# Kernel tuning notes

Hardware: AMD Instinct MI355X
Metric: run time of the kernel (lower is better)

The kernel has to match this reference:

```python
import jax, jax.numpy as jnp
import numpy as np
import math

N = 50000
E = 500000
IN_C = 128
T_FEAT = 16
OUT_C = 128
EPS = 1e-5
NEG_SLOPE = 0.01


def setup_inputs() -> dict:
    key = jax.random.key(0)
    ks = jax.random.split(key, 10)
    x = jax.random.normal(ks[0], (N, IN_C), dtype=jnp.float32)
    edge_index = jax.random.randint(ks[1], (2, E), 0, N, dtype=jnp.int64)
    edge_weight = jax.random.uniform(ks[2], (E,), dtype=jnp.float32)
    time_diff = jax.random.uniform(ks[3], (1,), dtype=jnp.float32)
    d_in = IN_C + T_FEAT
    morning_freq = jax.random.normal(ks[4], (T_FEAT,), dtype=jnp.float32)
    W_gcn = jax.random.normal(ks[5], (d_in, OUT_C), dtype=jnp.float32) / np.sqrt(d_in)
    b_gcn = jnp.zeros((OUT_C,), dtype=jnp.float32)
    gamma = jnp.ones((OUT_C,), dtype=jnp.float32)
    beta = jnp.zeros((OUT_C,), dtype=jnp.float32)
    W_lin = jax.random.normal(ks[6], (OUT_C, OUT_C), dtype=jnp.float32) / np.sqrt(OUT_C)
    b_lin = jax.random.normal(ks[7], (OUT_C,), dtype=jnp.float32) * 0.01
    return {"x": x, "edge_index": edge_index, "edge_weight": edge_weight,
            "time_diff": time_diff, "morning_freq": morning_freq,
            "W_gcn": W_gcn, "b_gcn": b_gcn, "gamma": gamma, "beta": beta,
            "W_lin": W_lin, "b_lin": b_lin}


def _gcn_conv(h, edge_index, edge_weight):
    # PyG GCNConv aggregation: add self-loops (weight 1), symmetric normalization.
    row, col = edge_index[0], edge_index[1]
    loop = jnp.arange(N, dtype=edge_index.dtype)
    row_f = jnp.concatenate([row, loop])
    col_f = jnp.concatenate([col, loop])
    ew_f = jnp.concatenate([edge_weight, jnp.ones((N,), dtype=h.dtype)])
    deg = jax.ops.segment_sum(ew_f, col_f, num_segments=N)
    dinv = jnp.where(deg > 0, jax.lax.rsqrt(jnp.maximum(deg, 1e-12)), 0.0)
    norm = dinv[row_f] * ew_f * dinv[col_f]                 # [E+N]
    msg = h[row_f] * norm[:, None]                          # gather + scale
    return jax.ops.segment_sum(msg, col_f, num_segments=N)  # scatter-add


def reference(x, edge_index, edge_weight, time_diff, morning_freq,
              W_gcn, b_gcn, gamma, beta, W_lin, b_lin):
    td = time_diff[0]
    # time_segment == 'morning_peak': sin encoding, tiled over all nodes
    enc = jnp.sin(td * morning_freq * math.pi)              # [T]
    enc = jnp.broadcast_to(enc[None, :], (x.shape[0], T_FEAT))
    h = jnp.concatenate([x, enc], axis=1)                   # [N, in+T]
    h = h @ W_gcn                                           # GCN linear transform
    h = _gcn_conv(h, edge_index, edge_weight) + b_gcn       # [N, out]
    # BatchNorm1d (training-mode batch statistics, biased variance)
    mean = jnp.mean(h, axis=0)
    var = jnp.mean(jnp.square(h - mean), axis=0)
    h = gamma * (h - mean) * jax.lax.rsqrt(var + EPS) + beta
    h = jnp.where(h >= 0, h, NEG_SLOPE * h)                 # LeakyReLU
    h = h @ W_lin + b_lin                                   # Linear (dropout=eval identity)
    return h
```

## Files before the change

### kernel.cpp

```cpp
#include <hip/hip_runtime.h>
#include <hip/hip_bf16.h>

#define NN 50000
#define NE 500000
#define C 128
#define NBLK ((NN + 255) / 256)
#define HISTB ((NE + 255) / 256)
#define SPB (NN / 8)
#define RB 128
#define RROWS ((SPB + RB - 1) / RB)
#define GB ((NN + 63) / 64)
#define BN_EPS 1e-5f
#define NEG 0.01f
#define WSCALE 16777216.0f
#define WMASK  0xFFFFFFFFFFFULL

typedef __attribute__((ext_vector_type(8))) short bf16x8;
typedef __attribute__((ext_vector_type(4))) float f32x4;

__device__ inline unsigned short f2bf(float f) {
    unsigned int u = __float_as_uint(f);
    unsigned int r = (u + 0x7fffu + ((u >> 16) & 1u)) >> 16;
    return (unsigned short)r;
}
__device__ inline unsigned int pack2(float a, float b) {
    return (unsigned int)f2bf(a) | ((unsigned int)f2bf(b) << 16);
}
__device__ inline float4 bf4_to_f4(uint2 u) {
    float4 r;
    r.x = __uint_as_float(u.x << 16);
    r.y = __uint_as_float(u.x & 0xffff0000u);
    r.z = __uint_as_float(u.y << 16);
    r.w = __uint_as_float(u.y & 0xffff0000u);
    return r;
}

__global__ __launch_bounds__(256) void setup_kernel(const float* __restrict__ Wg,
                                                    const float* __restrict__ Wl,
                                                    unsigned int* __restrict__ Wgt,
                                                    unsigned int* __restrict__ Wlt,
                                                    const float* __restrict__ td,
                                                    const float* __restrict__ mf,
                                                    float* __restrict__ cvec,
                                                    float* __restrict__ zreg) {
    const int b = blockIdx.x;
    const int t = threadIdx.x;
    if (b < 128) {
        long i = (long)b * 256 + t;
        const long n = 2L * NN + 4;
        const long s = 128L * 256;
        for (; i < n; i += s) zreg[i] = 0.f;
    } else if (b == 128) {
        const int col = t >> 1;
        const int half = t & 1;
        for (int j = 0; j < 32; j++) {
            int ku = half * 32 + j;
            int k0 = 2 * ku;
            unsigned int g = (unsigned int)((ku >> 2) ^ (col & 15));
            unsigned int slot = (unsigned int)col * 64u + (g << 2) + (unsigned int)(ku & 3);
            Wgt[slot] = pack2(Wg[(size_t)k0 * C + col], Wg[(size_t)(k0 + 1) * C + col]);
            Wlt[slot] = pack2(Wl[(size_t)k0 * C + col], Wl[(size_t)(k0 + 1) * C + col]);
        }
    } else {
        if (t < 128) {
            float tv = td[0];
            float acc = 0.f;
#pragma unroll
            for (int j = 0; j < 16; j++) {
                float s = sinf(tv * mf[j] * 3.14159265358979323846f);
                acc = fmaf(s, Wg[(128 + j) * C + t], acc);
            }
            cvec[t] = acc;
        }
    }
}

__global__ void hist_kernel(const int* __restrict__ ei, const float* __restrict__ ew,
                            unsigned long long* __restrict__ hist, int* __restrict__ rank) {
    int e = blockIdx.x * blockDim.x + threadIdx.x;
    if (e < NE) {
        int c = ei[NE + e];
        unsigned long long pack = (1ULL << 44) | (unsigned long long)(ew[e] * WSCALE);
        unsigned long long old = atomicAdd(&hist[c], pack);
        rank[e] = (int)(old >> 44);
    }
}

__global__ __launch_bounds__(256) void gemm1_kernel(const float* __restrict__ X,
                                                    const unsigned int* __restrict__ Wt,
                                                    const float* __restrict__ cvec,
                                                    unsigned short* __restrict__ Hb) {
    __shared__ unsigned int wsh[8192];
    const int t = threadIdx.x;
#pragma unroll
    for (int i = 0; i < 8; i++)
        ((uint4*)wsh)[t + i * 256] = ((const uint4*)Wt)[t + i * 256];

    const int lane = t & 63;
    const int wid = t >> 6;
    const int lrow = lane & 15;
    const int kb = lane >> 4;
    const int row = blockIdx.x * 64 + wid * 16 + lrow;
    const float* xrow = X + (size_t)min(row, NN - 1) * C;

    f32x4 acc[8];
#pragma unroll
    for (int n = 0; n < 8; n++) acc[n] = (f32x4){0.f, 0.f, 0.f, 0.f};
    __syncthreads();

#pragma unroll
    for (int ks = 0; ks < 4; ks++) {
        float4 a0 = *(const float4*)(xrow + ks * 32 + kb * 8);
        float4 a1 = *(const float4*)(xrow + ks * 32 + kb * 8 + 4);
        union { unsigned int u[4]; bf16x8 v; } af;
        af.u[0] = pack2(a0.x, a0.y); af.u[1] = pack2(a0.z, a0.w);
        af.u[2] = pack2(a1.x, a1.y); af.u[3] = pack2(a1.z, a1.w);
        const unsigned int gp = (unsigned int)((ks * 4 + kb) ^ lrow);
#pragma unroll
        for (int n = 0; n < 8; n++) {
            int col = n * 16 + lrow;
            union { uint4 q; bf16x8 v; } bfm;
            bfm.q = *(const uint4*)&wsh[col * 64 + gp * 4];
            acc[n] = __builtin_amdgcn_mfma_f32_16x16x32_bf16(af.v, bfm.v, acc[n], 0, 0, 0);
        }
    }
    const int orow = blockIdx.x * 64 + wid * 16 + kb * 4;
#pragma unroll
    for (int n = 0; n < 8; n++) {
        int col = n * 16 + lrow;
        float cv = cvec[col];
#pragma unroll
        for (int i = 0; i < 4; i++) {
            int r = orow + i;
            if (r < NN) Hb[(size_t)r * C + col] = f2bf(acc[n][i] + cv);
        }
    }
}

__global__ __launch_bounds__(256) void scanp1_kernel(const unsigned long long* __restrict__ hist,
                                                     int* __restrict__ rptr,
                                                     int* __restrict__ bsum) {
    __shared__ int s[256];
    const int t = threadIdx.x;
    const int i = blockIdx.x * 256 + t;
    int v = (i < NN) ? (int)(hist[i] >> 44) : 0;
    s[t] = v;
    __syncthreads();
    for (int off = 1; off < 256; off <<= 1) {
        int add = (t >= off) ? s[t - off] : 0;
        __syncthreads();
        s[t] += add;
        __syncthreads();
    }
    if (i < NN) rptr[i] = s[t] - v;
    if (t == 255) bsum[blockIdx.x] = s[255];
}

__global__ __launch_bounds__(256) void scanp3_kernel(int* __restrict__ rptr,
                                                     const int* __restrict__ bsum,
                                                     const unsigned long long* __restrict__ hist,
                                                     float* __restrict__ dinv) {
    __shared__ int sb[256];
    const int t = threadIdx.x;
    const int b = blockIdx.x;
    sb[t] = (t < NBLK && t < b) ? bsum[t] : 0;
    __syncthreads();
    for (int off = 128; off > 0; off >>= 1) {
        if (t < off) sb[t] += sb[t + off];
        __syncthreads();
    }
    const int boff = sb[0];
    const int i = b * 256 + t;
    if (i < NN) {
        rptr[i] += boff;
        float degw = (float)(hist[i] & WMASK) * (1.0f / WSCALE);
        dinv[i] = rsqrtf(degw + 1.0f);
    }
    if (b == 0 && t == 0) rptr[NN] = NE;
}

__global__ void fill_kernel(const int* __restrict__ ei, const float* __restrict__ ew,
                            const float* __restrict__ dinv, const int* __restrict__ rptr,
                            const int* __restrict__ rank, int2* __restrict__ csr) {
    int e = blockIdx.x * blockDim.x + threadIdx.x;
    if (e >= NE) return;
    int r = ei[e], c = ei[NE + e];
    int slot = rptr[c] + rank[e];
    float w = dinv[r] * ew[e] * dinv[c];
    csr[slot] = make_int2(r, __float_as_int(w));
}

__global__ __launch_bounds__(256) void spmm_kernel(const int* __restrict__ rptr,
                                                   const int2* __restrict__ csr,
                                                   const unsigned short* __restrict__ Hb,
                                                   const float* __restrict__ dinv,
                                                   const float* __restrict__ bg,
                                                   float* __restrict__ OUT,
                                                   float* __restrict__ P) {
    const int nl = threadIdx.x >> 5;
    const int lane = threadIdx.x & 31;
    const int node = blockIdx.x * 8 + nl;
    const int ch = lane * 4;
    int s = rptr[node], e = rptr[node + 1];
    float d = dinv[node];
    float dd = d * d;
    float4 h = bf4_to_f4(*(const uint2*)(Hb + (size_t)node * C + ch));
    float4 acc = make_float4(dd * h.x, dd * h.y, dd * h.z, dd * h.w);
    float4 accB = make_float4(0.f, 0.f, 0.f, 0.f);
    int j = s;
    for (; j + 4 <= e; j += 4) {
        int2 e0 = csr[j], e1 = csr[j + 1], e2 = csr[j + 2], e3 = csr[j + 3];
        float w0 = __int_as_float(e0.y), w1 = __int_as_float(e1.y);
        float w2 = __int_as_float(e2.y), w3 = __int_as_float(e3.y);
        uint2 u0 = *(const uint2*)(Hb + (size_t)e0.x * C + ch);
        uint2 u1 = *(const uint2*)(Hb + (size_t)e1.x * C + ch);
        uint2 u2 = *(const uint2*)(Hb + (size_t)e2.x * C + ch);
        uint2 u3 = *(const uint2*)(Hb + (size_t)e3.x * C + ch);
        float4 v0 = bf4_to_f4(u0), v1 = bf4_to_f4(u1), v2 = bf4_to_f4(u2), v3 = bf4_to_f4(u3);
        acc.x = fmaf(v0.x, w0, acc.x);  acc.y = fmaf(v0.y, w0, acc.y);
        acc.z = fmaf(v0.z, w0, acc.z);  acc.w = fmaf(v0.w, w0, acc.w);
        accB.x = fmaf(v1.x, w1, accB.x); accB.y = fmaf(v1.y, w1, accB.y);
        accB.z = fmaf(v1.z, w1, accB.z); accB.w = fmaf(v1.w, w1, accB.w);
        acc.x = fmaf(v2.x, w2, acc.x);  acc.y = fmaf(v2.y, w2, acc.y);
        acc.z = fmaf(v2.z, w2, acc.z);  acc.w = fmaf(v2.w, w2, acc.w);
        accB.x = fmaf(v3.x, w3, accB.x); accB.y = fmaf(v3.y, w3, accB.y);
        accB.z = fmaf(v3.z, w3, accB.z); accB.w = fmaf(v3.w, w3, accB.w);
    }
    for (; j < e; j++) {
        int2 e0 = csr[j];
        float w0 = __int_as_float(e0.y);
        float4 v0 = bf4_to_f4(*(const uint2*)(Hb + (size_t)e0.x * C + ch));
        acc.x = fmaf(v0.x, w0, acc.x); acc.y = fmaf(v0.y, w0, acc.y);
        acc.z = fmaf(v0.z, w0, acc.z); acc.w = fmaf(v0.w, w0, acc.w);
    }
    acc.x += accB.x; acc.y += accB.y; acc.z += accB.z; acc.w += accB.w;
    float4 b = *(const float4*)(bg + ch);
    acc.x += b.x; acc.y += b.y; acc.z += b.z; acc.w += b.w;
    *(float4*)(OUT + (size_t)node * C + ch) = acc;

    __shared__ __align__(16) float4 sred[2][8][32];
    float4 sq = make_float4(acc.x * acc.x, acc.y * acc.y, acc.z * acc.z, acc.w * acc.w);
    sred[0][nl][lane] = acc;
    sred[1][nl][lane] = sq;
    __syncthreads();
    if (nl == 0) {
        float4 s0 = sred[0][0][lane], q0 = sred[1][0][lane];
#pragma unroll
        for (int k = 1; k < 8; k++) {
            float4 a = sred[0][k][lane];
            float4 q = sred[1][k][lane];
            s0.x += a.x; s0.y += a.y; s0.z += a.z; s0.w += a.w;
            q0.x += q.x; q0.y += q.y; q0.z += q.z; q0.w += q.w;
        }
        float* row = P + (size_t)blockIdx.x * 256;
        *(float4*)(row + ch) = s0;
        *(float4*)(row + 128 + ch) = q0;
    }
}

__global__ __launch_bounds__(256) void reduce1_kernel(const float* __restrict__ P,
                                                      float* __restrict__ P2,
                                                      unsigned int* __restrict__ cnt,
                                                      const float* __restrict__ gm,
                                                      const float* __restrict__ bt,
                                                      float* __restrict__ sc,
                                                      float* __restrict__ sh) {
    const int c = threadIdx.x;
    const int r0 = blockIdx.x * RROWS;
    const int r1 = min(r0 + RROWS, SPB);
    float a0 = 0.f, a1 = 0.f, a2 = 0.f, a3 = 0.f;
    int r = r0;
    for (; r + 4 <= r1; r += 4) {
        a0 += P[(size_t)(r + 0) * 256 + c];
        a1 += P[(size_t)(r + 1) * 256 + c];
        a2 += P[(size_t)(r + 2) * 256 + c];
        a3 += P[(size_t)(r + 3) * 256 + c];
    }
    for (; r < r1; r++) a0 += P[(size_t)r * 256 + c];
    P2[(size_t)blockIdx.x * 256 + c] = (a0 + a1) + (a2 + a3);

    __threadfence();
    __shared__ unsigned int done;
    if (c == 0) done = atomicAdd(cnt, 1u);
    __syncthreads();
    if (done == RB - 1) {
        __threadfence();
        if (c < 128) {
            float s0 = 0.f, s1 = 0.f, q0 = 0.f, q1 = 0.f;
            for (int k = 0; k < RB; k += 2) {
                s0 += P2[(size_t)k * 256 + c];
                q0 += P2[(size_t)k * 256 + 128 + c];
                s1 += P2[(size_t)(k + 1) * 256 + c];
                q1 += P2[(size_t)(k + 1) * 256 + 128 + c];
            }
            float ssum = s0 + s1, ssq = q0 + q1;
            float mean = ssum / (float)NN;
            float var = ssq / (float)NN - mean * mean;
            var = fmaxf(var, 0.f);
            float rs = rsqrtf(var + BN_EPS);
            float s = gm[c] * rs;
            sc[c] = s;
            sh[c] = bt[c] - mean * s;
        }
    }
}

__global__ __launch_bounds__(256) void final_kernel(float* __restrict__ OUT,
                                                    const unsigned int* __restrict__ Wt,
                                                    const float* __restrict__ bl,
                                                    const float* __restrict__ sc,
                                                    const float* __restrict__ sh) {
    __shared__ unsigned int wsh[8192];
    const int t = threadIdx.x;
#pragma unroll
    for (int i = 0; i < 8; i++)
        ((uint4*)wsh)[t + i * 256] = ((const uint4*)Wt)[t + i * 256];

    const int lane = t & 63;
    const int wid = t >> 6;
    const int lrow = lane & 15;
    const int kb = lane >> 4;
    const int row = blockIdx.x * 64 + wid * 16 + lrow;
    const float* hrow = OUT + (size_t)min(row, NN - 1) * C;

    f32x4 acc[8];
#pragma unroll
    for (int n = 0; n < 8; n++) acc[n] = (f32x4){0.f, 0.f, 0.f, 0.f};
    __syncthreads();

#pragma unroll
    for (int ks = 0; ks < 4; ks++) {
        const int k0 = ks * 32 + kb * 8;
        float4 v0 = *(const float4*)(hrow + k0);
        float4 v1 = *(const float4*)(hrow + k0 + 4);
        float4 s0 = *(const float4*)(sc + k0);
        float4 s1 = *(const float4*)(sc + k0 + 4);
        float4 h0 = *(const float4*)(sh + k0);
        float4 h1 = *(const float4*)(sh + k0 + 4);
        float a[8];
        a[0] = fmaf(v0.x, s0.x, h0.x); a[1] = fmaf(v0.y, s0.y, h0.y);
        a[2] = fmaf(v0.z, s0.z, h0.z); a[3] = fmaf(v0.w, s0.w, h0.w);
        a[4] = fmaf(v1.x, s1.x, h1.x); a[5] = fmaf(v1.y, s1.y, h1.y);
        a[6] = fmaf(v1.z, s1.z, h1.z); a[7] = fmaf(v1.w, s1.w, h1.w);
#pragma unroll
        for (int i = 0; i < 8; i++) a[i] = a[i] >= 0.f ? a[i] : NEG * a[i];
        union { unsigned int u[4]; bf16x8 v; } af;
        af.u[0] = pack2(a[0], a[1]); af.u[1] = pack2(a[2], a[3]);
        af.u[2] = pack2(a[4], a[5]); af.u[3] = pack2(a[6], a[7]);
        const unsigned int gp = (unsigned int)((ks * 4 + kb) ^ lrow);
#pragma unroll
        for (int n = 0; n < 8; n++) {
            int col = n * 16 + lrow;
            union { uint4 q; bf16x8 v; } bfm;
            bfm.q = *(const uint4*)&wsh[col * 64 + gp * 4];
            acc[n] = __builtin_amdgcn_mfma_f32_16x16x32_bf16(af.v, bfm.v, acc[n], 0, 0, 0);
        }
    }
    const int orow = blockIdx.x * 64 + wid * 16 + kb * 4;
#pragma unroll
    for (int n = 0; n < 8; n++) {
        int col = n * 16 + lrow;
        float blv = bl[col];
#pragma unroll
        for (int i = 0; i < 4; i++) {
            int r = orow + i;
            if (r < NN) OUT[(size_t)r * C + col] = acc[n][i] + blv;
        }
    }
}

extern "C" void kernel_launch(void* const* d_in, const int* in_sizes, int n_in,
                              void* d_out, int out_size, void* d_ws, size_t ws_size,
                              hipStream_t stream) {
    const float* x  = (const float*)d_in[0];
    const int*   ei = (const int*)d_in[1];
    const float* ew = (const float*)d_in[2];
    const float* td = (const float*)d_in[3];
    const float* mf = (const float*)d_in[4];
    const float* Wg = (const float*)d_in[5];
    const float* bg = (const float*)d_in[6];
    const float* gm = (const float*)d_in[7];
    const float* bt = (const float*)d_in[8];
    const float* Wl = (const float*)d_in[9];
    const float* bl = (const float*)d_in[10];
    float* out = (float*)d_out;

    unsigned short* h1b = (unsigned short*)d_ws;
    unsigned long long* hist = (unsigned long long*)(h1b + (size_t)NN * C);
    unsigned int* cnt = (unsigned int*)(hist + NN);
    float* dinv   = (float*)(cnt + 4);
    float* cvec   = dinv + NN;
    float* sc     = cvec + C;
    float* sh     = sc + C;
    int*   rptr   = (int*)(sh + C);
    int*   bsum   = rptr + NN + 8;
    int*   rank   = bsum + NBLK + 12;
    int2*  csr    = (int2*)(rank + NE);
    float* P      = (float*)(csr + NE);
    float* P2     = P + (size_t)SPB * 256;
    unsigned int* Wgt = (unsigned int*)(P2 + RB * 256);
    unsigned int* Wlt = Wgt + 8192;

    setup_kernel<<<130, 256, 0, stream>>>(Wg, Wl, Wgt, Wlt, td, mf, cvec, (float*)hist);
    hist_kernel<<<HISTB, 256, 0, stream>>>(ei, ew, hist, rank);
    gemm1_kernel<<<GB, 256, 0, stream>>>(x, Wgt, cvec, h1b);
    scanp1_kernel<<<NBLK, 256, 0, stream>>>(hist, rptr, bsum);
    scanp3_kernel<<<NBLK, 256, 0, stream>>>(rptr, bsum, hist, dinv);
    fill_kernel<<<HISTB, 256, 0, stream>>>(ei, ew, dinv, rptr, rank, csr);
    spmm_kernel<<<SPB, 256, 0, stream>>>(rptr, csr, h1b, dinv, bg, out, P);
    reduce1_kernel<<<RB, 256, 0, stream>>>(P, P2, cnt, gm, bt, sc, sh);
    final_kernel<<<GB, 256, 0, stream>>>(out, Wlt, bl, sc, sh);
}
```

Measured before the change: 145.8 us.

## Store aggregated features in bf16, widen SpMM lanes, fuse scan kernels

```diff
diff --git a/kernel.cpp b/kernel.cpp
--- a/kernel.cpp
+++ b/kernel.cpp
@@ -6,9 +6,9 @@
 #define C 128
 #define NBLK ((NN + 255) / 256)
 #define HISTB ((NE + 255) / 256)
-#define SPB (NN / 8)
+#define SPB2 (NN / 16)
 #define RB 128
-#define RROWS ((SPB + RB - 1) / RB)
+#define RROWS ((SPB2 + RB - 1) / RB)
 #define GB ((NN + 63) / 64)
 #define BN_EPS 1e-5f
 #define NEG 0.01f
@@ -17,6 +17,7 @@
 
 typedef __attribute__((ext_vector_type(8))) short bf16x8;
 typedef __attribute__((ext_vector_type(4))) float f32x4;
+typedef unsigned long long ull;
 
 __device__ inline unsigned short f2bf(float f) {
     unsigned int u = __float_as_uint(f);
@@ -26,12 +27,12 @@
 __device__ inline unsigned int pack2(float a, float b) {
     return (unsigned int)f2bf(a) | ((unsigned int)f2bf(b) << 16);
 }
-__device__ inline float4 bf4_to_f4(uint2 u) {
+__device__ inline float4 bf4_to_f4(unsigned int lo, unsigned int hi) {
     float4 r;
-    r.x = __uint_as_float(u.x << 16);
-    r.y = __uint_as_float(u.x & 0xffff0000u);
-    r.z = __uint_as_float(u.y << 16);
-    r.w = __uint_as_float(u.y & 0xffff0000u);
+    r.x = __uint_as_float(lo << 16);
+    r.y = __uint_as_float(lo & 0xffff0000u);
+    r.z = __uint_as_float(hi << 16);
+    r.w = __uint_as_float(hi & 0xffff0000u);
     return r;
 }
 
@@ -47,7 +48,7 @@
     const int t = threadIdx.x;
     if (b < 128) {
         long i = (long)b * 256 + t;
-        const long n = 2L * NN + 4;
+        const long n = 2L * NN + 516;
         const long s = 128L * 256;
         for (; i < n; i += s) zreg[i] = 0.f;
     } else if (b == 128) {
@@ -76,12 +77,12 @@
 }
 
 __global__ void hist_kernel(const int* __restrict__ ei, const float* __restrict__ ew,
-                            unsigned long long* __restrict__ hist, int* __restrict__ rank) {
+                            ull* __restrict__ hist, int* __restrict__ rank) {
     int e = blockIdx.x * blockDim.x + threadIdx.x;
     if (e < NE) {
         int c = ei[NE + e];
-        unsigned long long pack = (1ULL << 44) | (unsigned long long)(ew[e] * WSCALE);
-        unsigned long long old = atomicAdd(&hist[c], pack);
+        ull pack = (1ULL << 44) | (ull)(ew[e] * WSCALE);
+        ull old = atomicAdd(&hist[c], pack);
         rank[e] = (int)(old >> 44);
     }
 }
@@ -137,13 +138,17 @@
     }
 }
 
-__global__ __launch_bounds__(256) void scanp1_kernel(const unsigned long long* __restrict__ hist,
-                                                     int* __restrict__ rptr,
-                                                     int* __restrict__ bsum) {
+__global__ __launch_bounds__(256) void scan_kernel(const ull* __restrict__ hist,
+                                                   int* __restrict__ rptr,
+                                                   float* __restrict__ dinv,
+                                                   ull* __restrict__ bflag) {
     __shared__ int s[256];
+    __shared__ int pre[256];
     const int t = threadIdx.x;
-    const int i = blockIdx.x * 256 + t;
-    int v = (i < NN) ? (int)(hist[i] >> 44) : 0;
+    const int b = blockIdx.x;
+    const int i = b * 256 + t;
+    ull hv = (i < NN) ? hist[i] : 0ULL;
+    int v = (int)(hv >> 44);
     s[t] = v;
     __syncthreads();
     for (int off = 1; off < 256; off <<= 1) {
@@ -152,28 +157,27 @@
         s[t] += add;
         __syncthreads();
     }
-    if (i < NN) rptr[i] = s[t] - v;
-    if (t == 255) bsum[blockIdx.x] = s[255];
-}
-
-__global__ __launch_bounds__(256) void scanp3_kernel(int* __restrict__ rptr,
-                                                     const int* __restrict__ bsum,
-                                                     const unsigned long long* __restrict__ hist,
-                                                     float* __restrict__ dinv) {
-    __shared__ int sb[256];
-    const int t = threadIdx.x;
-    const int b = blockIdx.x;
-    sb[t] = (t < NBLK && t < b) ? bsum[t] : 0;
+    if (t == 255)
+        __hip_atomic_store(&bflag[b], (1ULL << 32) | (ull)(unsigned int)s[255],
+                           __ATOMIC_RELEASE, __HIP_MEMORY_SCOPE_AGENT);
+    int pv = 0;
+    if (t < b) {
+        ull f;
+        do {
+            f = __hip_atomic_load(&bflag[t], __ATOMIC_ACQUIRE, __HIP_MEMORY_SCOPE_AGENT);
+        } while (!(f >> 32));
+        pv = (int)(unsigned int)f;
+    }
+    pre[t] = pv;
     __syncthreads();
     for (int off = 128; off > 0; off >>= 1) {
-        if (t < off) sb[t] += sb[t + off];
+        if (t < off) pre[t] += pre[t + off];
         __syncthreads();
     }
-    const int boff = sb[0];
-    const int i = b * 256 + t;
+    const int boff = pre[0];
     if (i < NN) {
-        rptr[i] += boff;
-        float degw = (float)(hist[i] & WMASK) * (1.0f / WSCALE);
+        rptr[i] = boff + s[t] - v;
+        float degw = (float)(hv & WMASK) * (1.0f / WSCALE);
         dinv[i] = rsqrtf(degw + 1.0f);
     }
     if (b == 0 && t == 0) rptr[NN] = NE;
@@ -195,67 +199,87 @@
                                                    const unsigned short* __restrict__ Hb,
                                                    const float* __restrict__ dinv,
                                                    const float* __restrict__ bg,
-                                                   float* __restrict__ OUT,
+                                                   unsigned short* __restrict__ H2,
                                                    float* __restrict__ P) {
-    const int nl = threadIdx.x >> 5;
-    const int lane = threadIdx.x & 31;
-    const int node = blockIdx.x * 8 + nl;
-    const int ch = lane * 4;
-    int s = rptr[node], e = rptr[node + 1];
-    float d = dinv[node];
-    float dd = d * d;
-    float4 h = bf4_to_f4(*(const uint2*)(Hb + (size_t)node * C + ch));
-    float4 acc = make_float4(dd * h.x, dd * h.y, dd * h.z, dd * h.w);
-    float4 accB = make_float4(0.f, 0.f, 0.f, 0.f);
+    const int t = threadIdx.x;
+    const int nl = t >> 4;
+    const int lane = t & 15;
+    const int node = blockIdx.x * 16 + nl;
+    const int ch = lane * 8;
+    const int s = rptr[node], e = rptr[node + 1];
+    const float d = dinv[node];
+    const float dd = d * d;
+    uint4 hu = *(const uint4*)(Hb + (size_t)node * C + ch);
+    float4 hA = bf4_to_f4(hu.x, hu.y), hB = bf4_to_f4(hu.z, hu.w);
+    float4 aA = make_float4(dd * hA.x, dd * hA.y, dd * hA.z, dd * hA.w);
+    float4 aB = make_float4(dd * hB.x, dd * hB.y, dd * hB.z, dd * hB.w);
+    float4 bA = make_float4(0.f, 0.f, 0.f, 0.f);
+    float4 bB = make_float4(0.f, 0.f, 0.f, 0.f);
     int j = s;
     for (; j + 4 <= e; j += 4) {
-        int2 e0 = csr[j], e1 = csr[j + 1], e2 = csr[j + 2], e3 = csr[j + 3];
-        float w0 = __int_as_float(e0.y), w1 = __int_as_float(e1.y);
-        float w2 = __int_as_float(e2.y), w3 = __int_as_float(e3.y);
-        uint2 u0 = *(const uint2*)(Hb + (size_t)e0.x * C + ch);
-        uint2 u1 = *(const uint2*)(Hb + (size_t)e1.x * C + ch);
-        uint2 u2 = *(const uint2*)(Hb + (size_t)e2.x * C + ch);
-        uint2 u3 = *(const uint2*)(Hb + (size_t)e3.x * C + ch);
-        float4 v0 = bf4_to_f4(u0), v1 = bf4_to_f4(u1), v2 = bf4_to_f4(u2), v3 = bf4_to_f4(u3);
-        acc.x = fmaf(v0.x, w0, acc.x);  acc.y = fmaf(v0.y, w0, acc.y);
-        acc.z = fmaf(v0.z, w0, acc.z);  acc.w = fmaf(v0.w, w0, acc.w);
-        accB.x = fmaf(v1.x, w1, accB.x); accB.y = fmaf(v1.y, w1, accB.y);
-        accB.z = fmaf(v1.z, w1, accB.z); accB.w = fmaf(v1.w, w1, accB.w);
-        acc.x = fmaf(v2.x, w2, acc.x);  acc.y = fmaf(v2.y, w2, acc.y);
-        acc.z = fmaf(v2.z, w2, acc.z);  acc.w = fmaf(v2.w, w2, acc.w);
-        accB.x = fmaf(v3.x, w3, accB.x); accB.y = fmaf(v3.y, w3, accB.y);
-        accB.z = fmaf(v3.z, w3, accB.z); accB.w = fmaf(v3.w, w3, accB.w);
+        int2 m0 = csr[j], m1 = csr[j + 1], m2 = csr[j + 2], m3 = csr[j + 3];
+        uint4 u0 = *(const uint4*)(Hb + (size_t)m0.x * C + ch);
+        uint4 u1 = *(const uint4*)(Hb + (size_t)m1.x * C + ch);
+        uint4 u2 = *(const uint4*)(Hb + (size_t)m2.x * C + ch);
+        uint4 u3 = *(const uint4*)(Hb + (size_t)m3.x * C + ch);
+        float w0 = __int_as_float(m0.y), w1 = __int_as_float(m1.y);
+        float w2 = __int_as_float(m2.y), w3 = __int_as_float(m3.y);
+        float4 vA, vB;
+        vA = bf4_to_f4(u0.x, u0.y); vB = bf4_to_f4(u0.z, u0.w);
+        aA.x = fmaf(vA.x, w0, aA.x); aA.y = fmaf(vA.y, w0, aA.y);
+        aA.z = fmaf(vA.z, w0, aA.z); aA.w = fmaf(vA.w, w0, aA.w);
+        aB.x = fmaf(vB.x, w0, aB.x); aB.y = fmaf(vB.y, w0, aB.y);
+        aB.z = fmaf(vB.z, w0, aB.z); aB.w = fmaf(vB.w, w0, aB.w);
+        vA = bf4_to_f4(u1.x, u1.y); vB = bf4_to_f4(u1.z, u1.w);
+        bA.x = fmaf(vA.x, w1, bA.x); bA.y = fmaf(vA.y, w1, bA.y);
+        bA.z = fmaf(vA.z, w1, bA.z); bA.w = fmaf(vA.w, w1, bA.w);
+        bB.x = fmaf(vB.x, w1, bB.x); bB.y = fmaf(vB.y, w1, bB.y);
+        bB.z = fmaf(vB.z, w1, bB.z); bB.w = fmaf(vB.w, w1, bB.w);
+        vA = bf4_to_f4(u2.x, u2.y); vB = bf4_to_f4(u2.z, u2.w);
+        aA.x = fmaf(vA.x, w2, aA.x); aA.y = fmaf(vA.y, w2, aA.y);
+        aA.z = fmaf(vA.z, w2, aA.z); aA.w = fmaf(vA.w, w2, aA.w);
+        aB.x = fmaf(vB.x, w2, aB.x); aB.y = fmaf(vB.y, w2, aB.y);
+        aB.z = fmaf(vB.z, w2, aB.z); aB.w = fmaf(vB.w, w2, aB.w);
+        vA = bf4_to_f4(u3.x, u3.y); vB = bf4_to_f4(u3.z, u3.w);
+        bA.x = fmaf(vA.x, w3, bA.x); bA.y = fmaf(vA.y, w3, bA.y);
+        bA.z = fmaf(vA.z, w3, bA.z); bA.w = fmaf(vA.w, w3, bA.w);
+        bB.x = fmaf(vB.x, w3, bB.x); bB.y = fmaf(vB.y, w3, bB.y);
+        bB.z = fmaf(vB.z, w3, bB.z); bB.w = fmaf(vB.w, w3, bB.w);
     }
     for (; j < e; j++) {
-        int2 e0 = csr[j];
-        float w0 = __int_as_float(e0.y);
-        float4 v0 = bf4_to_f4(*(const uint2*)(Hb + (size_t)e0.x * C + ch));
-        acc.x = fmaf(v0.x, w0, acc.x); acc.y = fmaf(v0.y, w0, acc.y);
-        acc.z = fmaf(v0.z, w0, acc.z); acc.w = fmaf(v0.w, w0, acc.w);
-    }
-    acc.x += accB.x; acc.y += accB.y; acc.z += accB.z; acc.w += accB.w;
-    float4 b = *(const float4*)(bg + ch);
-    acc.x += b.x; acc.y += b.y; acc.z += b.z; acc.w += b.w;
-    *(float4*)(OUT + (size_t)node * C + ch) = acc;
-
-    __shared__ __align__(16) float4 sred[2][8][32];
-    float4 sq = make_float4(acc.x * acc.x, acc.y * acc.y, acc.z * acc.z, acc.w * acc.w);
-    sred[0][nl][lane] = acc;
-    sred[1][nl][lane] = sq;
-    __syncthreads();
-    if (nl == 0) {
-        float4 s0 = sred[0][0][lane], q0 = sred[1][0][lane];
-#pragma unroll
-        for (int k = 1; k < 8; k++) {
-            float4 a = sred[0][k][lane];
-            float4 q = sred[1][k][lane];
-            s0.x += a.x; s0.y += a.y; s0.z += a.z; s0.w += a.w;
-            q0.x += q.x; q0.y += q.y; q0.z += q.z; q0.w += q.w;
-        }
-        float* row = P + (size_t)blockIdx.x * 256;
-        *(float4*)(row + ch) = s0;
-        *(float4*)(row + 128 + ch) = q0;
-    }
+        int2 m0 = csr[j];
+        uint4 u0 = *(const uint4*)(Hb + (size_t)m0.x * C + ch);
+        float w0 = __int_as_float(m0.y);
+        float4 vA = bf4_to_f4(u0.x, u0.y), vB = bf4_to_f4(u0.z, u0.w);
+        aA.x = fmaf(vA.x, w0, aA.x); aA.y = fmaf(vA.y, w0, aA.y);
+        aA.z = fmaf(vA.z, w0, aA.z); aA.w = fmaf(vA.w, w0, aA.w);
+        aB.x = fmaf(vB.x, w0, aB.x); aB.y = fmaf(vB.y, w0, aB.y);
+        aB.z = fmaf(vB.z, w0, aB.z); aB.w = fmaf(vB.w, w0, aB.w);
+    }
+    aA.x += bA.x; aA.y += bA.y; aA.z += bA.z; aA.w += bA.w;
+    aB.x += bB.x; aB.y += bB.y; aB.z += bB.z; aB.w += bB.w;
+    float4 g0 = *(const float4*)(bg + ch);
+    float4 g1 = *(const float4*)(bg + ch + 4);
+    aA.x += g0.x; aA.y += g0.y; aA.z += g0.z; aA.w += g0.w;
+    aB.x += g1.x; aB.y += g1.y; aB.z += g1.z; aB.w += g1.w;
+    uint4 ou;
+    ou.x = pack2(aA.x, aA.y); ou.y = pack2(aA.z, aA.w);
+    ou.z = pack2(aB.x, aB.y); ou.w = pack2(aB.z, aB.w);
+    *(uint4*)(H2 + (size_t)node * C + ch) = ou;
+
+    __shared__ float sred[2][16][128];
+    *(float4*)&sred[0][nl][ch]     = aA;
+    *(float4*)&sred[0][nl][ch + 4] = aB;
+    float4 qA = make_float4(aA.x * aA.x, aA.y * aA.y, aA.z * aA.z, aA.w * aA.w);
+    float4 qB = make_float4(aB.x * aB.x, aB.y * aB.y, aB.z * aB.z, aB.w * aB.w);
+    *(float4*)&sred[1][nl][ch]     = qA;
+    *(float4*)&sred[1][nl][ch + 4] = qB;
+    __syncthreads();
+    const int q = t >> 7, c2 = t & 127;
+    float acc = 0.f;
+#pragma unroll
+    for (int k = 0; k < 16; k++) acc += sred[q][k][c2];
+    P[(size_t)blockIdx.x * 256 + t] = acc;
 }
 
 __global__ __launch_bounds__(256) void reduce1_kernel(const float* __restrict__ P,
@@ -267,7 +291,7 @@
                                                       float* __restrict__ sh) {
     const int c = threadIdx.x;
     const int r0 = blockIdx.x * RROWS;
-    const int r1 = min(r0 + RROWS, SPB);
+    const int r1 = min(r0 + RROWS, SPB2);
     float a0 = 0.f, a1 = 0.f, a2 = 0.f, a3 = 0.f;
     int r = r0;
     for (; r + 4 <= r1; r += 4) {
@@ -305,7 +329,8 @@
     }
 }
 
-__global__ __launch_bounds__(256) void final_kernel(float* __restrict__ OUT,
+__global__ __launch_bounds__(256) void final_kernel(const unsigned short* __restrict__ H2,
+                                                    float* __restrict__ OUT,
                                                     const unsigned int* __restrict__ Wt,
                                                     const float* __restrict__ bl,
                                                     const float* __restrict__ sc,
@@ -321,7 +346,7 @@
     const int lrow = lane & 15;
     const int kb = lane >> 4;
     const int row = blockIdx.x * 64 + wid * 16 + lrow;
-    const float* hrow = OUT + (size_t)min(row, NN - 1) * C;
+    const unsigned short* hrow = H2 + (size_t)min(row, NN - 1) * C;
 
     f32x4 acc[8];
 #pragma unroll
@@ -331,8 +356,9 @@
 #pragma unroll
     for (int ks = 0; ks < 4; ks++) {
         const int k0 = ks * 32 + kb * 8;
-        float4 v0 = *(const float4*)(hrow + k0);
-        float4 v1 = *(const float4*)(hrow + k0 + 4);
+        uint4 hu = *(const uint4*)(hrow + k0);
+        float4 v0 = bf4_to_f4(hu.x, hu.y);
+        float4 v1 = bf4_to_f4(hu.z, hu.w);
         float4 s0 = *(const float4*)(sc + k0);
         float4 s1 = *(const float4*)(sc + k0 + 4);
         float4 h0 = *(const float4*)(sh + k0);
@@ -386,28 +412,28 @@
     float* out = (float*)d_out;
 
     unsigned short* h1b = (unsigned short*)d_ws;
-    unsigned long long* hist = (unsigned long long*)(h1b + (size_t)NN * C);
+    unsigned short* h2b = h1b + (size_t)NN * C;
+    ull*   hist  = (ull*)(h2b + (size_t)NN * C);
     unsigned int* cnt = (unsigned int*)(hist + NN);
-    float* dinv   = (float*)(cnt + 4);
-    float* cvec   = dinv + NN;
-    float* sc     = cvec + C;
-    float* sh     = sc + C;
-    int*   rptr   = (int*)(sh + C);
-    int*   bsum   = rptr + NN + 8;
-    int*   rank   = bsum + NBLK + 12;
-    int2*  csr    = (int2*)(rank + NE);
-    float* P      = (float*)(csr + NE);
-    float* P2     = P + (size_t)SPB * 256;
+    ull*   bflag = (ull*)(cnt + 4);
+    float* dinv  = (float*)(bflag + 256);
+    float* cvec  = dinv + NN;
+    float* sc    = cvec + C;
+    float* sh    = sc + C;
+    int*   rptr  = (int*)(sh + C);
+    int*   rank  = rptr + NN + 8;
+    int2*  csr   = (int2*)(rank + NE);
+    float* P     = (float*)(csr + NE);
+    float* P2    = P + (size_t)SPB2 * 256;
     unsigned int* Wgt = (unsigned int*)(P2 + RB * 256);
     unsigned int* Wlt = Wgt + 8192;
 
     setup_kernel<<<130, 256, 0, stream>>>(Wg, Wl, Wgt, Wlt, td, mf, cvec, (float*)hist);
     hist_kernel<<<HISTB, 256, 0, stream>>>(ei, ew, hist, rank);
     gemm1_kernel<<<GB, 256, 0, stream>>>(x, Wgt, cvec, h1b);
-    scanp1_kernel<<<NBLK, 256, 0, stream>>>(hist, rptr, bsum);
-    scanp3_kernel<<<NBLK, 256, 0, stream>>>(rptr, bsum, hist, dinv);
+    scan_kernel<<<NBLK, 256, 0, stream>>>(hist, rptr, dinv, bflag);
     fill_kernel<<<HISTB, 256, 0, stream>>>(ei, ew, dinv, rptr, rank, csr);
-    spmm_kernel<<<SPB, 256, 0, stream>>>(rptr, csr, h1b, dinv, bg, out, P);
+    spmm_kernel<<<SPB2, 256, 0, stream>>>(rptr, csr, h1b, dinv, bg, h2b, P);
     reduce1_kernel<<<RB, 256, 0, stream>>>(P, P2, cnt, gm, bt, sc, sh);
-    final_kernel<<<GB, 256, 0, stream>>>(out, Wlt, bl, sc, sh);
-}
+    final_kernel<<<GB, 256, 0, stream>>>(h2b, out, Wlt, bl, sc, sh);
+}
```

New measurement: 142.7 us. 2.1% less time.
